# Kernel tuning notes

Hardware: AMD Instinct MI355X
Metric: run time of the kernel (lower is better)

## Reference

```python
import jax, jax.numpy as jnp
import numpy as np
import math

D_MODEL = 1024
N_HEADS = 16
HEAD_DIM = D_MODEL // N_HEADS  # 64
B, T = 2, 2048


def _rotate_half(x):
    x1, x2 = jnp.split(x, 2, axis=-1)
    return jnp.concatenate([-x2, x1], axis=-1)


def _rope_sin_cos(seq_len, dim, dtype=jnp.float32):
    # matches RotaryEmbedding: inv_freq over even indices, emb = [freqs, freqs]
    inv_freq = 1.0 / (10000.0 ** (jnp.arange(0, dim, 2, dtype=dtype) / dim))
    t = jnp.arange(seq_len, dtype=dtype)
    freqs = jnp.einsum('i,j->ij', t, inv_freq)          # [T, dim/2]
    emb = jnp.concatenate((freqs, freqs), axis=-1)      # [T, dim]
    sin = jnp.sin(emb)[None, :, None, :]                # [1, T, 1, dim]
    cos = jnp.cos(emb)[None, :, None, :]
    return sin, cos


def setup_inputs() -> dict:
    key = jax.random.key(0)
    k1, k2, k3 = jax.random.split(key, 3)
    x = jax.random.normal(k1, (B, T, D_MODEL), dtype=jnp.float32)
    # causal mask broadcast over batch and heads: [1, 1, T, T]
    mask = jnp.tril(jnp.ones((T, T), dtype=bool))[None, None]
    w_qkv = jax.random.normal(k2, (D_MODEL, 3 * D_MODEL), dtype=jnp.float32) / math.sqrt(D_MODEL)
    w_out = jax.random.normal(k3, (D_MODEL, D_MODEL), dtype=jnp.float32) / math.sqrt(D_MODEL)
    return {"x": x, "mask": mask, "w_qkv": w_qkv, "w_out": w_out}


def reference(x, mask, w_qkv, w_out):
    Bx, Tx, Dx = x.shape
    qkv = x @ w_qkv                                     # [B, T, 3D]
    q, k, v = jnp.split(qkv, 3, axis=-1)
    q = q.reshape(Bx, Tx, N_HEADS, HEAD_DIM)
    k = k.reshape(Bx, Tx, N_HEADS, HEAD_DIM)
    v = v.reshape(Bx, Tx, N_HEADS, HEAD_DIM)
    sin, cos = _rope_sin_cos(Tx, HEAD_DIM, x.dtype)
    q = q * cos + _rotate_half(q) * sin
    k = k * cos + _rotate_half(k) * sin
    scores = jnp.einsum('bthd,bThd->bhtT', q, k) / math.sqrt(HEAD_DIM)
    scores = jnp.where(mask, scores, -1e10)
    probs = jax.nn.softmax(scores, axis=-1)             # [B, H, T, T]
    out = jnp.einsum('bhtT,bThd->bthd', probs, v)
    out = out.reshape(Bx, Tx, Dx)
    return out @ w_out
```

## Files before the change

### kernel.cpp

```cpp
#include <hip/hip_runtime.h>
#include <math.h>

typedef unsigned short u16;
typedef __attribute__((ext_vector_type(8))) short short8;
typedef __attribute__((ext_vector_type(4))) float f32x4;

__device__ __forceinline__ u16 f2bf(float f) {
  unsigned int u = __float_as_uint(f);
  u += 0x7fffu + ((u >> 16) & 1u);
  return (u16)(u >> 16);
}
__device__ __forceinline__ float bf2f(u16 h) {
  return __uint_as_float(((unsigned int)h) << 16);
}

__device__ __forceinline__ f32x4 mfma16(short8 a, short8 b, f32x4 c) {
  return __builtin_amdgcn_mfma_f32_16x16x32_bf16(a, b, c, 0, 0, 0);
}

__device__ __forceinline__ unsigned cvtpk_bf16(float lo, float hi) {
  unsigned r;
  asm("v_cvt_pk_bf16_f32 %0, %1, %2" : "=v"(r) : "v"(lo), "v"(hi));
  return r;
}

#define NEG_BIG (-1e30f)

__device__ __forceinline__ void glds16(const u16* g, u16* l) {
  __builtin_amdgcn_global_load_lds(
      (const __attribute__((address_space(1))) unsigned int*)g,
      (__attribute__((address_space(3))) unsigned int*)l, 16, 0, 0);
}

__global__ __launch_bounds__(256) void detect_dtype3(const u16* __restrict__ a,
                                                     const u16* __restrict__ bb,
                                                     const u16* __restrict__ c,
                                                     int* __restrict__ flags) {
  const u16* x = (blockIdx.x == 0) ? a : (blockIdx.x == 1) ? bb : c;
  __shared__ int cnt;
  if (threadIdx.x == 0) cnt = 0;
  __syncthreads();
  int my = 0;
  for (int i = threadIdx.x; i < 4096; i += 256) {
    float v = bf2f(x[2 * i]);
    float av = fabsf(v);
    if (v == 0.0f || (av >= 1e-4f && av <= 100.0f)) my++;
  }
  atomicAdd(&cnt, my);
  __syncthreads();
  if (threadIdx.x == 0) flags[blockIdx.x] = (cnt > 2458) ? 1 : 0;
}

__global__ __launch_bounds__(256) void prep_all(const void* __restrict__ wqkv,
                                                const void* __restrict__ wout,
                                                const void* __restrict__ xin,
                                                u16* __restrict__ wqkvT,
                                                u16* __restrict__ woutT,
                                                u16* __restrict__ xb,
                                                float2* __restrict__ tab,
                                                const int* __restrict__ flags) {
  int z = blockIdx.z;
  int tid = threadIdx.x;
  if (z == 2) {
    if (blockIdx.x >= 16 || blockIdx.y >= 16) return;
    int idx = (blockIdx.y * 16 + blockIdx.x) * 256 + tid;
    int t = idx >> 5, d = idx & 31;
    float invf = expf(-(float)d * 0.28782313662425575f);
    float s, c;
    sincosf((float)t * invf, &s, &c);
    tab[idx] = make_float2(c, s);
    return;
  }
  if (z == 3) {
    bool isbf = (flags[0] != 0);
    int tg = (blockIdx.y * 48 + blockIdx.x) * 256 + tid;
    for (int i = tg; i < 524288; i += 196608) {
      int base = i * 8;
      if (isbf) {
        *(short8*)(xb + base) = *(const short8*)((const u16*)xin + base);
      } else {
        const float* xf = (const float*)xin;
        f32x4 x0 = *(const f32x4*)(xf + base);
        f32x4 x1 = *(const f32x4*)(xf + base + 4);
        short8 o;
#pragma unroll
        for (int u = 0; u < 4; ++u) { o[u] = (short)f2bf(x0[u]); o[u + 4] = (short)f2bf(x1[u]); }
        *(short8*)(xb + base) = o;
      }
    }
    return;
  }
  const void* in = (z == 0) ? wqkv : wout;
  u16* out = (z == 0) ? wqkvT : woutT;
  int C = (z == 0) ? 3072 : 1024;
  const int R = 1024;
  bool isbf = (flags[z + 1] != 0);
  if (z == 1 && blockIdx.x >= 16) return;
  __shared__ float tile[64][68];
  int tc = blockIdx.x * 64, tr = blockIdx.y * 64;
  int r = tid >> 3, cg = (tid & 7) << 3;
#pragma unroll
  for (int p = 0; p < 2; ++p) {
    int row = r + p * 32;
    if (isbf) {
      short8 v = *(const short8*)((const u16*)in + (size_t)(tr + row) * C + tc + cg);
#pragma unroll
      for (int u = 0; u < 8; ++u) tile[row][cg + u] = bf2f((u16)v[u]);
    } else {
      const float* inf = (const float*)in + (size_t)(tr + row) * C + tc + cg;
#pragma unroll
      for (int u = 0; u < 8; ++u) tile[row][cg + u] = inf[u];
    }
  }
  __syncthreads();
#pragma unroll
  for (int p = 0; p < 2; ++p) {
    int orow = r + p * 32;
    short8 v;
#pragma unroll
    for (int u = 0; u < 8; ++u) v[u] = (short)f2bf(tile[cg + u][orow]);
    *(short8*)(out + (size_t)(tc + orow) * R + tr + cg) = v;
  }
}

__device__ __forceinline__ void qkv_epilogue3(f32x4 acc[4][4], int bm, int bn,
                                              int wm, int wn, int quad, int lane15,
                                              int lane, const float2* __restrict__ tab,
                                              u16* Qo, u16* Ko, u16* VTo, u16* myE) {
  int nbase = bn + wn * 64;
  int h = (nbase & 1023) >> 6;
  if (nbase < 2048) {
    int l8 = lane15 & 7, lh = lane15 >> 3;
#pragma unroll
    for (int i = 0; i < 4; ++i) {
#pragma unroll
      for (int r = 0; r < 4; ++r) {
        int mloc = i * 16 + quad * 4 + r;
        int t = (bm + wm * 64 + mloc) & 2047;
        float2 cs0 = tab[t * 32 + lane15];
        float2 cs1 = tab[t * 32 + 16 + lane15];
        float v0 = acc[i][0][r], v1 = acc[i][1][r], v2 = acc[i][2][r], v3 = acc[i][3][r];
        int m7 = mloc & 7;
        u16* rowp = myE + mloc * 64 + l8;
        rowp[((0 + lh) ^ m7) * 8] = f2bf(v0 * cs0.x - v2 * cs0.y);
        rowp[((2 + lh) ^ m7) * 8] = f2bf(v1 * cs1.x - v3 * cs1.y);
        rowp[((4 + lh) ^ m7) * 8] = f2bf(v2 * cs0.x + v0 * cs0.y);
        rowp[((6 + lh) ^ m7) * 8] = f2bf(v3 * cs1.x + v1 * cs1.y);
      }
    }
    asm volatile("s_waitcnt lgkmcnt(0)" ::: "memory");
    u16* dst = (nbase < 1024) ? Qo : Ko;
#pragma unroll
    for (int p = 0; p < 8; ++p) {
      int f = p * 64 + lane;
      int mr = f >> 3, nc = f & 7;
      short8 val = *(const short8*)(myE + mr * 64 + (nc ^ (mr & 7)) * 8);
      int g = bm + wm * 64 + mr;
      int bI = g >> 11, tI = g & 2047;
      *(short8*)(dst + ((size_t)(bI * 16 + h) * 2048 + tI) * 64 + nc * 8) = val;
    }
  } else {
#pragma unroll
    for (int i = 0; i < 4; ++i)
#pragma unroll
      for (int j = 0; j < 4; ++j)
#pragma unroll
        for (int r = 0; r < 4; ++r) {
          int col = i * 16 + quad * 4 + r;
          int slot = (col >> 3) ^ (lane15 & 7);
          myE[(j * 16 + lane15) * 64 + slot * 8 + (col & 7)] = f2bf(acc[i][j][r]);
        }
    asm volatile("s_waitcnt lgkmcnt(0)" ::: "memory");
    int g0 = bm + wm * 64;
    int bI = g0 >> 11, t0 = g0 & 2047;
#pragma unroll
    for (int p = 0; p < 8; ++p) {
      int f = p * 64 + lane;
      int dr = f >> 3, tc = f & 7;
      short8 val = *(const short8*)(myE + dr * 64 + (tc ^ (dr & 7)) * 8);
      *(short8*)(VTo + ((size_t)(bI * 16 + h) * 64 + dr) * 2048 + t0 + tc * 8) = val;
    }
  }
}

__device__ __forceinline__ void stage256(const u16* __restrict__ X,
                                         const u16* __restrict__ WT,
                                         u16* lAq, u16* lBq,
                                         int bm, int bn, int k0, int tid) {
  const int K = 1024;
#pragma unroll
  for (int p = 0; p < 4; ++p) {
    int cid = p * 512 + tid;
    int r = cid >> 3;
    int cs = (cid & 7) ^ (r & 7);
    int dst = (cid & ~63) * 8;
    glds16(X + (size_t)(bm + r) * K + k0 + cs * 8, lAq + dst);
    glds16(WT + (size_t)(bn + r) * K + k0 + cs * 8, lBq + dst);
  }
}

__device__ __forceinline__ void qkv_step(const u16* lAq, const u16* lBq,
                                         f32x4 acc[8][4], int wm, int wn,
                                         int lane15, int quad) {
  short8 bfr[2][4];
#pragma unroll
  for (int j = 0; j < 4; ++j) {
    int row = wn * 64 + j * 16 + lane15;
    int ro = row * 64, r7 = row & 7;
    bfr[0][j] = *(const short8*)(lBq + ro + (quad ^ r7) * 8);
    bfr[1][j] = *(const short8*)(lBq + ro + ((4 + quad) ^ r7) * 8);
  }
#pragma unroll
  for (int qd = 0; qd < 4; ++qd) {
    short8 afr[2][2];
#pragma unroll
    for (int i2 = 0; i2 < 2; ++i2) {
      int row = wm * 128 + (qd * 2 + i2) * 16 + lane15;
      int ro = row * 64, r7 = row & 7;
      afr[i2][0] = *(const short8*)(lAq + ro + (quad ^ r7) * 8);
      afr[i2][1] = *(const short8*)(lAq + ro + ((4 + quad) ^ r7) * 8);
    }
    __builtin_amdgcn_s_setprio(1);
#pragma unroll
    for (int ks = 0; ks < 2; ++ks)
#pragma unroll
      for (int i2 = 0; i2 < 2; ++i2)
#pragma unroll
        for (int j = 0; j < 4; ++j)
          acc[qd * 2 + i2][j] = mfma16(afr[i2][ks], bfr[ks][j], acc[qd * 2 + i2][j]);
    __builtin_amdgcn_s_setprio(0);
  }
}

__global__ __launch_bounds__(512, 2) void gemm_qkv_256(const u16* __restrict__ X,
                                                       const u16* __restrict__ WT,
                                                       const float2* __restrict__ tab,
                                                       u16* __restrict__ Qo,
                                                       u16* __restrict__ Ko,
                                                       u16* __restrict__ VTo) {
  __shared__ u16 sh[65536];
  int tid = threadIdx.x;
  int wave = tid >> 6, lane = tid & 63;
  int lane15 = lane & 15, quad = lane >> 4;
  int wm = wave >> 2, wn = wave & 3;
  int swz = (blockIdx.x & 7) * 24 + (blockIdx.x >> 3);
  int bm = (swz / 12) * 256, bn = (swz % 12) * 256;
  f32x4 acc[8][4] = {};

  stage256(X, WT, sh, sh + 32768, bm, bn, 0, tid);

#pragma unroll 1
  for (int kt = 0; kt < 15; ++kt) {
    int q = kt & 1;
    stage256(X, WT, sh + (q ^ 1) * 16384, sh + 32768 + (q ^ 1) * 16384,
             bm, bn, (kt + 1) * 64, tid);
    asm volatile("s_waitcnt vmcnt(8)" ::: "memory");
    __builtin_amdgcn_sched_barrier(0);
    asm volatile("s_barrier" ::: "memory");
    qkv_step(sh + q * 16384, sh + 32768 + q * 16384, acc, wm, wn, lane15, quad);
    asm volatile("s_barrier" ::: "memory");
  }
  asm volatile("s_waitcnt vmcnt(0)" ::: "memory");
  __builtin_amdgcn_sched_barrier(0);
  asm volatile("s_barrier" ::: "memory");
  qkv_step(sh + 16384, sh + 32768 + 16384, acc, wm, wn, lane15, quad);
  __syncthreads();

  u16* myE = sh + wave * 8192;
  int nbase = bn + wn * 64;
  int h = (nbase & 1023) >> 6;
  if (nbase < 2048) {
    int l8 = lane15 & 7, lh = lane15 >> 3;
#pragma unroll
    for (int i = 0; i < 8; ++i) {
#pragma unroll
      for (int r = 0; r < 4; ++r) {
        int mloc = i * 16 + quad * 4 + r;
        int t = (bm + wm * 128 + mloc) & 2047;
        float2 cs0 = tab[t * 32 + lane15];
        float2 cs1 = tab[t * 32 + 16 + lane15];
        float v0 = acc[i][0][r], v1 = acc[i][1][r], v2 = acc[i][2][r], v3 = acc[i][3][r];
        int m7 = mloc & 7;
        u16* rowp = myE + mloc * 64 + l8;
        rowp[((0 + lh) ^ m7) * 8] = f2bf(v0 * cs0.x - v2 * cs0.y);
        rowp[((2 + lh) ^ m7) * 8] = f2bf(v1 * cs1.x - v3 * cs1.y);
        rowp[((4 + lh) ^ m7) * 8] = f2bf(v2 * cs0.x + v0 * cs0.y);
        rowp[((6 + lh) ^ m7) * 8] = f2bf(v3 * cs1.x + v1 * cs1.y);
      }
    }
    asm volatile("s_waitcnt lgkmcnt(0)" ::: "memory");
    u16* dst = (nbase < 1024) ? Qo : Ko;
#pragma unroll
    for (int p = 0; p < 16; ++p) {
      int f = p * 64 + lane;
      int mr = f >> 3, nc = f & 7;
      short8 val = *(const short8*)(myE + mr * 64 + (nc ^ (mr & 7)) * 8);
      int g = bm + wm * 128 + mr;
      int bI = g >> 11, tI = g & 2047;
      *(short8*)(dst + ((size_t)(bI * 16 + h) * 2048 + tI) * 64 + nc * 8) = val;
    }
  } else {
#pragma unroll
    for (int i = 0; i < 8; ++i)
#pragma unroll
      for (int j = 0; j < 4; ++j)
#pragma unroll
        for (int r = 0; r < 4; ++r) {
          int col = i * 16 + quad * 4 + r;
          int slot = (col >> 3) ^ (lane15 & 7);
          myE[(j * 16 + lane15) * 128 + slot * 8 + (col & 7)] = f2bf(acc[i][j][r]);
        }
    asm volatile("s_waitcnt lgkmcnt(0)" ::: "memory");
    int g0 = bm + wm * 128;
    int bI = g0 >> 11, t0 = g0 & 2047;
#pragma unroll
    for (int p = 0; p < 16; ++p) {
      int f = p * 64 + lane;
      int dr = f >> 4, tc = f & 15;
      short8 val = *(const short8*)(myE + dr * 128 + (tc ^ (dr & 7)) * 8);
      *(short8*)(VTo + ((size_t)(bI * 16 + h) * 64 + dr) * 2048 + t0 + tc * 8) = val;
    }
  }
}

__global__ __launch_bounds__(256) void gemm_qkv_rope(const void* __restrict__ Xv,
                                                     const u16* __restrict__ WT,
                                                     const float2* __restrict__ tab,
                                                     u16* __restrict__ Qo,
                                                     u16* __restrict__ Ko,
                                                     u16* __restrict__ VTo,
                                                     const int* __restrict__ flag) {
  const int K = 1024;
  __shared__ u16 buf[16384];
  u16* lA = buf;
  u16* lB = buf + 5120;
  bool isbf = (*flag != 0);
  int tid = threadIdx.x;
  int wave = tid >> 6, lane = tid & 63;
  int lane15 = lane & 15, quad = lane >> 4;
  int wm = wave >> 1, wn = wave & 1;
  int bm = blockIdx.x * 128, bn = blockIdx.y * 128;
  int sr = tid >> 2, scg = (tid & 3) << 3;
  f32x4 acc[4][4] = {};
  for (int k0 = 0; k0 < K; k0 += 32) {
    __syncthreads();
#pragma unroll
    for (int p = 0; p < 2; ++p) {
      int row = sr + p * 64;
      if (isbf) {
        *(short8*)(lA + row * 40 + scg) =
            *(const short8*)((const u16*)Xv + (size_t)(bm + row) * K + k0 + scg);
      } else {
        const float* xf = (const float*)Xv + (size_t)(bm + row) * K + k0 + scg;
        f32x4 x0 = *(const f32x4*)(xf);
        f32x4 x1 = *(const f32x4*)(xf + 4);
        short8 o;
#pragma unroll
        for (int u = 0; u < 4; ++u) { o[u] = (short)f2bf(x0[u]); o[u + 4] = (short)f2bf(x1[u]); }
        *(short8*)(lA + row * 40 + scg) = o;
      }
      *(short8*)(lB + row * 40 + scg) = *(const short8*)(WT + (size_t)(bn + row) * K + k0 + scg);
    }
    __syncthreads();
    short8 af[4], bf[4];
#pragma unroll
    for (int i = 0; i < 4; ++i)
      af[i] = *(const short8*)(lA + (wm * 64 + i * 16 + lane15) * 40 + quad * 8);
#pragma unroll
    for (int j = 0; j < 4; ++j)
      bf[j] = *(const short8*)(lB + (wn * 64 + j * 16 + lane15) * 40 + quad * 8);
#pragma unroll
    for (int i = 0; i < 4; ++i)
#pragma unroll
      for (int j = 0; j < 4; ++j)
        acc[i][j] = mfma16(af[i], bf[j], acc[i][j]);
  }
  __syncthreads();
  qkv_epilogue3(acc, bm, bn, wm, wn, quad, lane15, lane, tab, Qo, Ko, VTo,
                buf + wave * 4096);
}

__device__ __forceinline__ short8 lds_frag(const u16* buf, int row, int chunk) {
  int s = chunk ^ (row & 7);
  return *(const short8*)(buf + row * 64 + s * 8);
}

__device__ __forceinline__ void stage_tile(const u16* gK, const u16* gV,
                                           u16* lK, u16* lV, int wave, int lane) {
#pragma unroll
  for (int p = 0; p < 2; ++p) {
    int f = (p * 4 + wave) * 64 + lane;
    int r = f >> 3;
    int c = (f & 7) ^ (r & 7);
    glds16(gK + (size_t)r * 64 + c * 8, lK + (p * 4 + wave) * 512);
    glds16(gV + (size_t)r * 2048 + c * 8, lV + (p * 4 + wave) * 512);
  }
}

__global__ __launch_bounds__(256, 4) void attn_fused(const u16* __restrict__ Q,
                                                     const u16* __restrict__ K,
                                                     const u16* __restrict__ VT,
                                                     u16* __restrict__ Ao) {
  int bx = blockIdx.x;
  int bh = bx & 31;
  int a = bx >> 5;
  int b = bh >> 4, h = bh & 15;
  int tid = threadIdx.x, wave = tid >> 6, lane = tid & 63;
  int lane15 = lane & 15, quad = lane >> 4;
  const u16* Qb = Q + (size_t)bh * 2048 * 64;
  const u16* Kb = K + (size_t)bh * 2048 * 64;
  const u16* Vb = VT + (size_t)bh * 64 * 2048;

  __shared__ u16 Kl[2][64 * 64];
  __shared__ u16 Vl[2][64 * 64];
  __shared__ u16 lP[4][16 * 64];
  u16* myP = lP[wave];
  int l7 = lane15 & 7, lh = lane15 >> 3;

#pragma unroll 1
  for (int ph = 0; ph < 2; ++ph) {
    int qt = ph ? (31 - a) : a;
    int q0 = qt * 64 + wave * 16;

    short8 qf0 = *(const short8*)(Qb + (size_t)(q0 + lane15) * 64 + quad * 8);
    short8 qf1 = *(const short8*)(Qb + (size_t)(q0 + lane15) * 64 + 32 + quad * 8);

    f32x4 Ov[4] = {};
    float tsum[4] = {0.f, 0.f, 0.f, 0.f};

    int ntiles = qt + 1;
    __syncthreads();
    stage_tile(Kb, Vb, Kl[0], Vl[0], wave, lane);

    for (int kt = 0; kt < ntiles; ++kt) {
      int kbase = kt * 64;
      int cur = kt & 1;
      __syncthreads();
      if (kt + 1 < ntiles)
        stage_tile(Kb + (size_t)(kbase + 64) * 64, Vb + kbase + 64,
                   Kl[cur ^ 1], Vl[cur ^ 1], wave, lane);

      f32x4 S[4];
#pragma unroll
      for (int j = 0; j < 4; ++j) {
        short8 k0 = lds_frag(Kl[cur], j * 16 + lane15, quad);
        short8 k1 = lds_frag(Kl[cur], j * 16 + lane15, 4 + quad);
        f32x4 z = {};
        z = mfma16(qf0, k0, z);
        z = mfma16(qf1, k1, z);
        S[j] = z;
      }
      if (kt == qt) {
#pragma unroll
        for (int j = 0; j < 4; ++j) {
          int kpos = kbase + j * 16 + lane15;
#pragma unroll
          for (int r = 0; r < 4; ++r)
            if (kpos > q0 + quad * 4 + r) S[j][r] = NEG_BIG;
        }
      }
#pragma unroll
      for (int j = 0; j < 4; ++j)
#pragma unroll
        for (int r = 0; r < 4; ++r) {
          float p = __expf(fmaf(S[j][r], 0.125f, -8.0f));
          S[j][r] = p;
          tsum[r] += p;
        }
#pragma unroll
      for (int j = 0; j < 4; ++j) {
        unsigned pk01 = cvtpk_bf16(S[j][0], S[j][1]);
        unsigned pk23 = cvtpk_bf16(S[j][2], S[j][3]);
#pragma unroll
        for (int r = 0; r < 4; ++r) {
          int lrow = quad * 4 + r;
          int slot = (j * 2 + lh) ^ (lrow & 7);
          unsigned v = (r < 2) ? pk01 : pk23;
          myP[lrow * 64 + slot * 8 + l7] = (r & 1) ? (u16)(v >> 16) : (u16)v;
        }
      }
      asm volatile("s_waitcnt lgkmcnt(0)" ::: "memory");
      short8 pa0 = *(const short8*)(myP + lane15 * 64 + ((quad) ^ l7) * 8);
      short8 pa1 = *(const short8*)(myP + lane15 * 64 + ((4 + quad) ^ l7) * 8);
#pragma unroll
      for (int j = 0; j < 4; ++j) {
        short8 v0 = lds_frag(Vl[cur], j * 16 + lane15, quad);
        short8 v1 = lds_frag(Vl[cur], j * 16 + lane15, 4 + quad);
        Ov[j] = mfma16(pa0, v0, Ov[j]);
        Ov[j] = mfma16(pa1, v1, Ov[j]);
      }
    }
    float rl[4];
#pragma unroll
    for (int r = 0; r < 4; ++r) {
      float v = tsum[r];
      v += __shfl_xor(v, 1);
      v += __shfl_xor(v, 2);
      v += __shfl_xor(v, 4);
      v += __shfl_xor(v, 8);
      rl[r] = 1.f / v;
    }
#pragma unroll
    for (int j = 0; j < 4; ++j)
#pragma unroll
      for (int r = 0; r < 4; ++r) {
        int t = q0 + quad * 4 + r;
        Ao[(size_t)(b * 2048 + t) * 1024 + h * 64 + j * 16 + lane15] =
            f2bf(Ov[j][r] * rl[r]);
      }
  }
}

__global__ __launch_bounds__(256) void gemm_out(const u16* __restrict__ A,
                                                const u16* __restrict__ WT,
                                                float* __restrict__ out) {
  const int K = 1024;
  __shared__ u16 lA[64 * 128];
  __shared__ u16 lB[128 * 128];
  int tid = threadIdx.x;
  int wave = tid >> 6, lane = tid & 63;
  int lane15 = lane & 15, quad = lane >> 4;
  int wm = wave >> 1, wn = wave & 1;
  int bm = blockIdx.x * 64, bn = blockIdx.y * 128;
  f32x4 acc[2][4] = {};
  for (int k0 = 0; k0 < K; k0 += 128) {
    __syncthreads();
#pragma unroll
    for (int p = 0; p < 4; ++p) {
      int g = p * 4 + wave;
      int f = g * 64 + lane;
      int r = f >> 4;
      int c16 = (f & 15) ^ (r & 15);
      glds16(A + (size_t)(bm + r) * K + k0 + c16 * 8, lA + g * 512);
    }
#pragma unroll
    for (int p = 0; p < 8; ++p) {
      int g = p * 4 + wave;
      int f = g * 64 + lane;
      int r = f >> 4;
      int c16 = (f & 15) ^ (r & 15);
      glds16(WT + (size_t)(bn + r) * K + k0 + c16 * 8, lB + g * 512);
    }
    __syncthreads();
#pragma unroll
    for (int ks = 0; ks < 4; ++ks) {
      int so = ((ks * 4 + quad) ^ lane15) * 8;
      short8 af[2], bf[4];
#pragma unroll
      for (int i = 0; i < 2; ++i)
        af[i] = *(const short8*)(lA + (wm * 32 + i * 16 + lane15) * 128 + so);
#pragma unroll
      for (int j = 0; j < 4; ++j)
        bf[j] = *(const short8*)(lB + (wn * 64 + j * 16 + lane15) * 128 + so);
#pragma unroll
      for (int i = 0; i < 2; ++i)
#pragma unroll
        for (int j = 0; j < 4; ++j)
          acc[i][j] = mfma16(af[i], bf[j], acc[i][j]);
    }
  }
#pragma unroll
  for (int i = 0; i < 2; ++i)
#pragma unroll
    for (int r = 0; r < 4; ++r) {
      int m = bm + wm * 32 + i * 16 + quad * 4 + r;
      size_t rowo = (size_t)m * 1024 + bn + wn * 64 + lane15;
      out[rowo] = acc[i][0][r];
      out[rowo + 16] = acc[i][1][r];
      out[rowo + 32] = acc[i][2][r];
      out[rowo + 48] = acc[i][3][r];
    }
}

__global__ void ws_sentinel(float* out, float val) {
  if (threadIdx.x == 0) out[1] = val;
}

extern "C" void kernel_launch(void* const* d_in, const int* in_sizes, int n_in,
                              void* d_out, int out_size, void* d_ws, size_t ws_size,
                              hipStream_t stream) {
  (void)out_size;
  const void* x = nullptr;
  const void* w_qkv = nullptr;
  const void* w_out = nullptr;
  for (int i = 0; i < n_in; ++i) {
    if (in_sizes[i] == 4194304 && !x) x = d_in[i];
    else if (in_sizes[i] == 3145728 && !w_qkv) w_qkv = d_in[i];
    else if (in_sizes[i] == 1048576 && !w_out) w_out = d_in[i];
  }
  float* out = (float*)d_out;

  const size_t EL_B = 32 + 4194304 + 1048576 + 3 * 4194304 + 262144;
  const size_t REQ_B = EL_B * 2;
  const size_t REQ_A = (EL_B + 4194304) * 2;
  if (ws_size < REQ_B) {
    ws_sentinel<<<1, 64, 0, stream>>>(out, 1.0e6f + 1000.0f * (float)(ws_size >> 20));
    return;
  }
  int* flags = (int*)d_ws;
  u16* base = (u16*)d_ws + 32;
  u16* wqkvT = base;
  u16* attnw = base;
  u16* woutT = base + 4194304;
  u16* Qw = woutT + 1048576;
  u16* Kw = Qw + 4194304;
  u16* VTw = Kw + 4194304;
  float2* tab = (float2*)(VTw + 4194304);
  u16* xb = VTw + 4194304 + 262144;

  detect_dtype3<<<3, 256, 0, stream>>>((const u16*)x, (const u16*)w_qkv,
                                       (const u16*)w_out, flags);
  if (ws_size >= REQ_A) {
    prep_all<<<dim3(48, 16, 4), 256, 0, stream>>>(w_qkv, w_out, x, wqkvT, woutT,
                                                  xb, tab, flags);
    gemm_qkv_256<<<dim3(192), dim3(512), 0, stream>>>(xb, wqkvT, tab, Qw, Kw, VTw);
  } else {
    prep_all<<<dim3(48, 16, 3), 256, 0, stream>>>(w_qkv, w_out, x, wqkvT, woutT,
                                                  nullptr, tab, flags);
    gemm_qkv_rope<<<dim3(32, 24), 256, 0, stream>>>(x, wqkvT, tab, Qw, Kw, VTw, flags + 0);
  }
  attn_fused<<<512, 256, 0, stream>>>(Qw, Kw, VTw, attnw);
  gemm_out<<<dim3(64, 8), 256, 0, stream>>>(attnw, woutT, out);
}
```

Measured before the change: 198.1 us.

## Rewrite attention kernel with 32x32 MFMA, register P exchange, 128-row query blocks

Switches the fused causal attention kernel from 16x16x32 to 32x32x16 bf16 MFMA. S is computed transposed (K as A operand), so P can be repacked into the PV operand with cross-half lane shuffles instead of a per-wave LDS round trip. Each block now covers 128 query rows (32 per wave) in a single pass over its K/V tiles, replacing the old two-phase pairing of 64-row tiles. Waves whose rows lie above a K tile skip it. The cost is higher register pressure (occupancy hint cut from 4 to 2), and causal work is less evenly balanced across waves inside a block.

New measurement: 214.7 us. +8.4%, slower.

```diff
diff --git a/kernel.cpp b/kernel.cpp
--- a/kernel.cpp
+++ b/kernel.cpp
@@ -4,6 +4,8 @@
 typedef unsigned short u16;
 typedef __attribute__((ext_vector_type(8))) short short8;
 typedef __attribute__((ext_vector_type(4))) float f32x4;
+typedef __attribute__((ext_vector_type(16))) float f32x16;
+typedef __attribute__((ext_vector_type(4))) unsigned uint4v;
 
 __device__ __forceinline__ u16 f2bf(float f) {
   unsigned int u = __float_as_uint(f);
@@ -17,11 +19,22 @@
 __device__ __forceinline__ f32x4 mfma16(short8 a, short8 b, f32x4 c) {
   return __builtin_amdgcn_mfma_f32_16x16x32_bf16(a, b, c, 0, 0, 0);
 }
+__device__ __forceinline__ f32x16 mfma32(short8 a, short8 b, f32x16 c) {
+  return __builtin_amdgcn_mfma_f32_32x32x16_bf16(a, b, c, 0, 0, 0);
+}
 
 __device__ __forceinline__ unsigned cvtpk_bf16(float lo, float hi) {
   unsigned r;
   asm("v_cvt_pk_bf16_f32 %0, %1, %2" : "=v"(r) : "v"(lo), "v"(hi));
   return r;
+}
+
+__device__ __forceinline__ void xchg32(unsigned x, unsigned y, int hi,
+                                       unsigned& a, unsigned& b) {
+  unsigned xs = (unsigned)__shfl_xor((int)x, 32);
+  unsigned ys = (unsigned)__shfl_xor((int)y, 32);
+  a = hi ? ys : x;
+  b = hi ? y : xs;
 }
 
 #define NEG_BIG (-1e30f)
@@ -397,117 +410,103 @@
   }
 }
 
-__global__ __launch_bounds__(256, 4) void attn_fused(const u16* __restrict__ Q,
+__global__ __launch_bounds__(256, 2) void attn_fused(const u16* __restrict__ Q,
                                                      const u16* __restrict__ K,
                                                      const u16* __restrict__ VT,
                                                      u16* __restrict__ Ao) {
   int bx = blockIdx.x;
   int bh = bx & 31;
   int a = bx >> 5;
+  int g = (a & 1) ? (15 - (a >> 1)) : (a >> 1);
   int b = bh >> 4, h = bh & 15;
   int tid = threadIdx.x, wave = tid >> 6, lane = tid & 63;
-  int lane15 = lane & 15, quad = lane >> 4;
+  int l31 = lane & 31, hi = lane >> 5;
+  int q0w = g * 128 + wave * 32;
   const u16* Qb = Q + (size_t)bh * 2048 * 64;
   const u16* Kb = K + (size_t)bh * 2048 * 64;
   const u16* Vb = VT + (size_t)bh * 64 * 2048;
 
   __shared__ u16 Kl[2][64 * 64];
   __shared__ u16 Vl[2][64 * 64];
-  __shared__ u16 lP[4][16 * 64];
-  u16* myP = lP[wave];
-  int l7 = lane15 & 7, lh = lane15 >> 3;
+
+  short8 qb[4];
+#pragma unroll
+  for (int c = 0; c < 4; ++c)
+    qb[c] = *(const short8*)(Qb + (size_t)(q0w + l31) * 64 + c * 16 + hi * 8);
+
+  f32x16 Od0 = {}, Od1 = {};
+  float ts[4] = {0.f, 0.f, 0.f, 0.f};
+
+  int ntiles = 2 * g + 2;
+  stage_tile(Kb, Vb, Kl[0], Vl[0], wave, lane);
 
 #pragma unroll 1
-  for (int ph = 0; ph < 2; ++ph) {
-    int qt = ph ? (31 - a) : a;
-    int q0 = qt * 64 + wave * 16;
-
-    short8 qf0 = *(const short8*)(Qb + (size_t)(q0 + lane15) * 64 + quad * 8);
-    short8 qf1 = *(const short8*)(Qb + (size_t)(q0 + lane15) * 64 + 32 + quad * 8);
-
-    f32x4 Ov[4] = {};
-    float tsum[4] = {0.f, 0.f, 0.f, 0.f};
-
-    int ntiles = qt + 1;
+  for (int kt = 0; kt < ntiles; ++kt) {
+    int kbase = kt * 64;
+    int cur = kt & 1;
     __syncthreads();
-    stage_tile(Kb, Vb, Kl[0], Vl[0], wave, lane);
-
-    for (int kt = 0; kt < ntiles; ++kt) {
-      int kbase = kt * 64;
-      int cur = kt & 1;
-      __syncthreads();
-      if (kt + 1 < ntiles)
-        stage_tile(Kb + (size_t)(kbase + 64) * 64, Vb + kbase + 64,
-                   Kl[cur ^ 1], Vl[cur ^ 1], wave, lane);
-
-      f32x4 S[4];
-#pragma unroll
-      for (int j = 0; j < 4; ++j) {
-        short8 k0 = lds_frag(Kl[cur], j * 16 + lane15, quad);
-        short8 k1 = lds_frag(Kl[cur], j * 16 + lane15, 4 + quad);
-        f32x4 z = {};
-        z = mfma16(qf0, k0, z);
-        z = mfma16(qf1, k1, z);
-        S[j] = z;
-      }
-      if (kt == qt) {
-#pragma unroll
-        for (int j = 0; j < 4; ++j) {
-          int kpos = kbase + j * 16 + lane15;
-#pragma unroll
-          for (int r = 0; r < 4; ++r)
-            if (kpos > q0 + quad * 4 + r) S[j][r] = NEG_BIG;
+    if (kt + 1 < ntiles)
+      stage_tile(Kb + (size_t)(kbase + 64) * 64, Vb + kbase + 64,
+                 Kl[cur ^ 1], Vl[cur ^ 1], wave, lane);
+
+    if (kbase <= q0w + 31) {
+      bool diag = (kbase + 63 > q0w);
+#pragma unroll
+      for (int s = 0; s < 2; ++s) {
+        f32x16 st = {};
+#pragma unroll
+        for (int c = 0; c < 4; ++c) {
+          short8 ka = lds_frag(Kl[cur], s * 32 + l31, c * 2 + hi);
+          st = mfma32(ka, qb[c], st);
+        }
+        float p[16];
+#pragma unroll
+        for (int reg = 0; reg < 16; ++reg) {
+          int klocal = (reg & 3) + 8 * (reg >> 2) + 4 * hi;
+          float pv = __expf(fmaf(st[reg], 0.125f, -8.0f));
+          if (diag && (kbase + s * 32 + klocal > q0w + l31)) pv = 0.f;
+          p[reg] = pv;
+          ts[reg & 3] += pv;
+        }
+        unsigned w01 = cvtpk_bf16(p[0], p[1]);
+        unsigned w23 = cvtpk_bf16(p[2], p[3]);
+        unsigned w45 = cvtpk_bf16(p[4], p[5]);
+        unsigned w67 = cvtpk_bf16(p[6], p[7]);
+        unsigned w89 = cvtpk_bf16(p[8], p[9]);
+        unsigned wab = cvtpk_bf16(p[10], p[11]);
+        unsigned wcd = cvtpk_bf16(p[12], p[13]);
+        unsigned wef = cvtpk_bf16(p[14], p[15]);
+        unsigned a0, a1, a2, a3, c0, c1, c2, c3;
+        xchg32(w01, w45, hi, a0, a2);
+        xchg32(w23, w67, hi, a1, a3);
+        xchg32(w89, wcd, hi, c0, c2);
+        xchg32(wab, wef, hi, c1, c3);
+        union UU { uint4v u; short8 s8; };
+        UU u0; u0.u = (uint4v){a0, a1, a2, a3};
+        UU u1; u1.u = (uint4v){c0, c1, c2, c3};
+        short8 pa[2] = {u0.s8, u1.s8};
+#pragma unroll
+        for (int t = 0; t < 2; ++t) {
+          int kchunk = s * 4 + t * 2 + hi;
+          short8 vb0 = lds_frag(Vl[cur], l31, kchunk);
+          Od0 = mfma32(pa[t], vb0, Od0);
+          short8 vb1 = lds_frag(Vl[cur], 32 + l31, kchunk);
+          Od1 = mfma32(pa[t], vb1, Od1);
         }
       }
-#pragma unroll
-      for (int j = 0; j < 4; ++j)
-#pragma unroll
-        for (int r = 0; r < 4; ++r) {
-          float p = __expf(fmaf(S[j][r], 0.125f, -8.0f));
-          S[j][r] = p;
-          tsum[r] += p;
-        }
-#pragma unroll
-      for (int j = 0; j < 4; ++j) {
-        unsigned pk01 = cvtpk_bf16(S[j][0], S[j][1]);
-        unsigned pk23 = cvtpk_bf16(S[j][2], S[j][3]);
-#pragma unroll
-        for (int r = 0; r < 4; ++r) {
-          int lrow = quad * 4 + r;
-          int slot = (j * 2 + lh) ^ (lrow & 7);
-          unsigned v = (r < 2) ? pk01 : pk23;
-          myP[lrow * 64 + slot * 8 + l7] = (r & 1) ? (u16)(v >> 16) : (u16)v;
-        }
-      }
-      asm volatile("s_waitcnt lgkmcnt(0)" ::: "memory");
-      short8 pa0 = *(const short8*)(myP + lane15 * 64 + ((quad) ^ l7) * 8);
-      short8 pa1 = *(const short8*)(myP + lane15 * 64 + ((4 + quad) ^ l7) * 8);
-#pragma unroll
-      for (int j = 0; j < 4; ++j) {
-        short8 v0 = lds_frag(Vl[cur], j * 16 + lane15, quad);
-        short8 v1 = lds_frag(Vl[cur], j * 16 + lane15, 4 + quad);
-        Ov[j] = mfma16(pa0, v0, Ov[j]);
-        Ov[j] = mfma16(pa1, v1, Ov[j]);
-      }
-    }
-    float rl[4];
-#pragma unroll
-    for (int r = 0; r < 4; ++r) {
-      float v = tsum[r];
-      v += __shfl_xor(v, 1);
-      v += __shfl_xor(v, 2);
-      v += __shfl_xor(v, 4);
-      v += __shfl_xor(v, 8);
-      rl[r] = 1.f / v;
-    }
-#pragma unroll
-    for (int j = 0; j < 4; ++j)
-#pragma unroll
-      for (int r = 0; r < 4; ++r) {
-        int t = q0 + quad * 4 + r;
-        Ao[(size_t)(b * 2048 + t) * 1024 + h * 64 + j * 16 + lane15] =
-            f2bf(Ov[j][r] * rl[r]);
-      }
+    }
+  }
+  float tsum = (ts[0] + ts[1]) + (ts[2] + ts[3]);
+  float fsum = tsum + __shfl_xor(tsum, 32);
+  float rl = 1.f / fsum;
+#pragma unroll
+  for (int reg = 0; reg < 16; ++reg) {
+    int qp = (reg & 3) + 8 * (reg >> 2) + 4 * hi;
+    float r = __shfl(rl, qp);
+    int t = q0w + qp;
+    size_t rowo = (size_t)(b * 2048 + t) * 1024 + h * 64;
+    Ao[rowo + l31] = f2bf(Od0[reg] * r);
+    Ao[rowo + 32 + l31] = f2bf(Od1[reg] * r);
   }
 }
 
```
